# Kernel tuning notes

Measured on AMD Instinct MI355X. Metric: run time of the kernel, lower is better.

Reference implementation:

```python
import jax, jax.numpy as jnp
import numpy as np

B, S, D, HEADS = 2, 1024, 1024, 16
DK = D // HEADS           # 64: size of the 'heads' axis after split (namedtensor quirk)
LOW = D // DK             # 16: size of the contracted 'lower' axis
SCALE = float(D)          # Attention(p, scale=d_model) -> divide by d_model
NEG = -1.0e9


def setup_inputs() -> dict:
    key = jax.random.key(0)
    ks = jax.random.split(key, 8)
    query = jax.random.normal(ks[0], (B, S, D), dtype=jnp.float32)
    key_t = jax.random.normal(ks[1], (B, S, D), dtype=jnp.float32)
    value = jax.random.normal(ks[2], (B, S, D), dtype=jnp.float32)
    mask = jax.random.bernoulli(ks[3], 0.25, (B, S, S))  # True -> masked out
    std = 1.0 / np.sqrt(D)
    Wq = jax.random.normal(ks[4], (D, D), dtype=jnp.float32) * std
    Wk = jax.random.normal(ks[5], (D, D), dtype=jnp.float32) * std
    Wv = jax.random.normal(ks[6], (D, D), dtype=jnp.float32) * std
    Wo = jax.random.normal(ks[7], (D, D), dtype=jnp.float32) * std
    return {"query": query, "key": key_t, "value": value, "mask": mask,
            "Wq": Wq, "Wk": Wk, "Wv": Wv, "Wo": Wo}


def reference(query, key, value, mask, Wq, Wk, Wv, Wo):
    # nn.Linear(d_model, d_model, bias=False): y = x @ W.T
    def split(x, W):
        y = jnp.einsum('bsd,ed->bse', x, W)
        return y.reshape(B, -1, DK, LOW)  # hidden -> ('heads'=DK, 'lower'=LOW)

    q = split(query, Wq)   # [B,Sq,H,L] with H=DK, L=LOW
    k = split(key, Wk)     # [B,Sk,H,L]
    v = split(value, Wv)   # [B,Sk,H,L]

    # scores = query.dot('lower', key) / d_model  -> contract the LOW axis
    scores = jnp.einsum('bqhl,bkhl->bhqk', q, k) / SCALE
    scores = jnp.where(mask[:, None, :, :], NEG, scores)  # scores[mask] = -1e9
    p_attn = jax.nn.softmax(scores, axis=-1)  # softmax over keys; dropout=eval

    # value.dot('keys', p_attn) -> [B,H,L,Q]; stack ('heads','lower') -> hidden
    x = jnp.einsum('bkhl,bhqk->bqhl', v, p_attn).reshape(B, -1, D)
    return jnp.einsum('bsd,ed->bse', x, Wo)
```

## Files before the change

### kernel.cpp

```cpp
#include <hip/hip_runtime.h>
#include <hip/hip_bf16.h>


typedef __hip_bfloat16 bf16;
typedef __attribute__((ext_vector_type(8))) short short8;
typedef __attribute__((ext_vector_type(4))) float f32x4;
typedef __attribute__((ext_vector_type(16))) float f32x16;

__device__ __forceinline__ unsigned short f2bf(float f) {
  union { float f; unsigned u; } x; x.f = f;
  unsigned r = x.u + 0x7FFFu + ((x.u >> 16) & 1u);
  return (unsigned short)(r >> 16);
}

__device__ __forceinline__ unsigned cvt_pk_bf16(float lo, float hi) {
  unsigned r;
  asm("v_cvt_pk_bf16_f32 %0, %1, %2" : "=v"(r) : "v"(lo), "v"(hi));
  return r;
}

__device__ __forceinline__ float fast_exp2(float x) {
#if __has_builtin(__builtin_amdgcn_exp2f)
  return __builtin_amdgcn_exp2f(x);
#else
  return __expf(x * 0.6931471805599453f);
#endif
}

__global__ void detect_mask(const unsigned char* __restrict__ m, int* __restrict__ flag) {
  const int i = blockIdx.x * 256 + threadIdx.x;
  const uchar4* p = (const uchar4*)m + (size_t)i * 4;
  unsigned any = 0;
#pragma unroll
  for (int j = 0; j < 4; ++j) { uchar4 v = p[j]; any |= (unsigned)v.y | (unsigned)v.z | (unsigned)v.w; }
  if (__ballot(any != 0)) { if ((threadIdx.x & 63) == 0) atomicOr(flag, 1); }
}

__global__ void bitpack_mask(const unsigned char* __restrict__ mB, const int* __restrict__ mI,
                             const int* __restrict__ flag, unsigned* __restrict__ out) {
  const int widx = blockIdx.x * 256 + threadIdx.x;
  const int row = widx >> 5, kb = widx & 31;
  unsigned bits = 0;
  if (*flag) {
    const uchar4* p = (const uchar4*)(mB + (size_t)row * 1024 + kb * 32);
#pragma unroll
    for (int j = 0; j < 8; ++j) {
      uchar4 v = p[j];
      bits |= ((unsigned)(v.x != 0) << (4 * j)) | ((unsigned)(v.y != 0) << (4 * j + 1))
            | ((unsigned)(v.z != 0) << (4 * j + 2)) | ((unsigned)(v.w != 0) << (4 * j + 3));
    }
  } else {
    const int4* p = (const int4*)(mI + (size_t)row * 1024 + kb * 32);
#pragma unroll
    for (int j = 0; j < 8; ++j) {
      int4 v = p[j];
      bits |= ((unsigned)(v.x != 0) << (4 * j)) | ((unsigned)(v.y != 0) << (4 * j + 1))
            | ((unsigned)(v.z != 0) << (4 * j + 2)) | ((unsigned)(v.w != 0) << (4 * j + 3));
    }
  }
  const int bq = row >> 10, qb = (row & 1023) >> 5, qr = row & 31;
  out[((((bq * 32 + qb) * 8 + (kb >> 2)) * 32 + qr) << 2) + (kb & 3)] = bits;
}

__global__ void convert_all(
    const float* __restrict__ s0, const float* __restrict__ s1, const float* __restrict__ s2,
    const float* __restrict__ s3, const float* __restrict__ s4, const float* __restrict__ s5,
    const float* __restrict__ s6,
    bf16* __restrict__ d0, bf16* __restrict__ d1, bf16* __restrict__ d2,
    bf16* __restrict__ d3, bf16* __restrict__ d4, bf16* __restrict__ d5,
    bf16* __restrict__ d6) {
  const int z = blockIdx.y;
  const float* s; bf16* d; int n8; float sc = 1.0f;
  if      (z == 0) { s = s0; d = d0; n8 = 262144; }
  else if (z == 1) { s = s1; d = d1; n8 = 262144; }
  else if (z == 2) { s = s2; d = d2; n8 = 262144; }
  else if (z == 3) { s = s3; d = d3; n8 = 131072; sc = 0.0014088818758681283f; }
  else if (z == 4) { s = s4; d = d4; n8 = 131072; }
  else if (z == 5) { s = s5; d = d5; n8 = 131072; }
  else             { s = s6; d = d6; n8 = 131072; }
  const int i = blockIdx.x * 256 + threadIdx.x;
  if (i >= n8) return;
  const f32x4* p = (const f32x4*)s + (size_t)i * 2;
  f32x4 a = p[0], b = p[1];
  uint4 o;
  o.x = cvt_pk_bf16(a[0] * sc, a[1] * sc); o.y = cvt_pk_bf16(a[2] * sc, a[3] * sc);
  o.z = cvt_pk_bf16(b[0] * sc, b[1] * sc); o.w = cvt_pk_bf16(b[2] * sc, b[3] * sc);
  ((uint4*)d)[i] = o;
}

#define GSTR 40

__global__ __launch_bounds__(256) void gemm_qkv(
    const bf16* __restrict__ A0, const bf16* __restrict__ A1, const bf16* __restrict__ A2,
    const bf16* __restrict__ W0, const bf16* __restrict__ W1, const bf16* __restrict__ W2,
    bf16* __restrict__ C0, bf16* __restrict__ C1, bf16* __restrict__ C2) {
  __shared__ __align__(16) char smem[64 * 136 * 2];
  bf16* As = (bf16*)smem;
  bf16* Bs = As + 128 * GSTR;
  const int z = blockIdx.z;
  const bf16* __restrict__ A = (z == 0) ? A0 : (z == 1) ? A1 : A2;
  const bf16* __restrict__ W = (z == 0) ? W0 : (z == 1) ? W1 : W2;
  bf16* __restrict__ C = (z == 0) ? C0 : (z == 1) ? C1 : C2;
  const int tid = threadIdx.x, lane = tid & 63, w = tid >> 6;
  const int wr = (w >> 1) * 64, wc = (w & 1) * 32;
  const int row0 = blockIdx.y * 128, col0 = blockIdx.x * 64;
  const int l15 = lane & 15, kg = lane >> 4;

  f32x4 acc[4][2];
#pragma unroll
  for (int m = 0; m < 4; ++m)
#pragma unroll
    for (int n = 0; n < 2; ++n)
#pragma unroll
      for (int j = 0; j < 4; ++j) acc[m][n][j] = 0.f;

  for (int k0 = 0; k0 < 1024; k0 += 32) {
    __syncthreads();
#pragma unroll
    for (int i = 0; i < 2; ++i) {
      const int idx = i * 256 + tid, r = idx >> 2, c = idx & 3;
      *(uint4*)(&As[r * GSTR + c * 8]) = *(const uint4*)(A + (size_t)(row0 + r) * 1024 + k0 + c * 8);
    }
    {
      const int r = tid >> 2, c = tid & 3;
      *(uint4*)(&Bs[r * GSTR + c * 8]) = *(const uint4*)(W + (size_t)(col0 + r) * 1024 + k0 + c * 8);
    }
    __syncthreads();
    short8 af[4], bfr[2];
#pragma unroll
    for (int m = 0; m < 4; ++m) af[m] = *(const short8*)(&As[(wr + m * 16 + l15) * GSTR + kg * 8]);
#pragma unroll
    for (int n = 0; n < 2; ++n) bfr[n] = *(const short8*)(&Bs[(wc + n * 16 + l15) * GSTR + kg * 8]);
#pragma unroll
    for (int m = 0; m < 4; ++m)
#pragma unroll
      for (int n = 0; n < 2; ++n)
        acc[m][n] = __builtin_amdgcn_mfma_f32_16x16x32_bf16(af[m], bfr[n], acc[m][n], 0, 0, 0);
  }

  const int bb = row0 >> 10, srel0 = row0 & 1023;
  if (z == 2) {
    bf16* T = (bf16*)smem;
    __syncthreads();
#pragma unroll
    for (int m = 0; m < 4; ++m)
#pragma unroll
      for (int n = 0; n < 2; ++n) {
        const int e = wc + n * 16 + l15;
        const int rb = wr + m * 16 + kg * 4;
        uint2 u;
        u.x = cvt_pk_bf16(acc[m][n][0], acc[m][n][1]);
        u.y = cvt_pk_bf16(acc[m][n][2], acc[m][n][3]);
        *(uint2*)(T + e * 136 + rb) = u;
      }
    __syncthreads();
#pragma unroll
    for (int i = 0; i < 4; ++i) {
      const int idx = i * 256 + tid;
      const int tile = idx >> 6, within = idx & 63;
      const int hl = tile >> 2, kbl = tile & 3;
      const int e_sub = within >> 2, kq4 = within & 3;
      uint4 v = *(const uint4*)(T + (hl * 16 + e_sub) * 136 + kbl * 32 + kq4 * 8);
      const int h = (col0 >> 4) + hl;
      const size_t kb = (size_t)((srel0 >> 5) + kbl);
      *(uint4*)((unsigned short*)C + (((size_t)(bb * 64 + h) * 32 + kb) * 512 + e_sub * 32 + kq4 * 8)) = v;
    }
  } else if (z == 1) {
#pragma unroll
    for (int m = 0; m < 4; ++m)
#pragma unroll
      for (int n = 0; n < 2; ++n) {
        const int ecol = wc + n * 16 + l15;
        const int h = (col0 >> 4) + (ecol >> 4), d = ecol & 15;
#pragma unroll
        for (int j = 0; j < 4; ++j) {
          const int s = srel0 + wr + m * 16 + kg * 4 + j;
          ((unsigned short*)C)[((size_t)(bb * 64 + h) * 32 + (s >> 5)) * 512 + (s & 31) * 16 + d] =
              f2bf(acc[m][n][j]);
        }
      }
  } else {
#pragma unroll
    for (int m = 0; m < 4; ++m)
#pragma unroll
      for (int n = 0; n < 2; ++n) {
        const int col = col0 + wc + n * 16 + l15;
#pragma unroll
        for (int j = 0; j < 4; ++j) {
          const int row = row0 + wr + m * 16 + kg * 4 + j;
          ((unsigned short*)C)[(size_t)row * 1024 + col] = f2bf(acc[m][n][j]);
        }
      }
  }
}

__global__ __launch_bounds__(256) void gemm_out(
    const bf16* __restrict__ A, const bf16* __restrict__ W, float* __restrict__ C) {
  __shared__ __align__(16) char smem[(128 + 64) * GSTR * 2];
  bf16* As = (bf16*)smem;
  bf16* Bs = As + 128 * GSTR;
  const int tid = threadIdx.x, lane = tid & 63, w = tid >> 6;
  const int wr = (w >> 1) * 64, wc = (w & 1) * 32;
  const int row0 = blockIdx.y * 128, col0 = blockIdx.x * 64;
  const int l15 = lane & 15, kg = lane >> 4;

  f32x4 acc[4][2];
#pragma unroll
  for (int m = 0; m < 4; ++m)
#pragma unroll
    for (int n = 0; n < 2; ++n)
#pragma unroll
      for (int j = 0; j < 4; ++j) acc[m][n][j] = 0.f;

  for (int k0 = 0; k0 < 1024; k0 += 32) {
    __syncthreads();
#pragma unroll
    for (int i = 0; i < 2; ++i) {
      const int idx = i * 256 + tid, r = idx >> 2, c = idx & 3;
      *(uint4*)(&As[r * GSTR + c * 8]) = *(const uint4*)(A + (size_t)(row0 + r) * 1024 + k0 + c * 8);
    }
    {
      const int r = tid >> 2, c = tid & 3;
      *(uint4*)(&Bs[r * GSTR + c * 8]) = *(const uint4*)(W + (size_t)(col0 + r) * 1024 + k0 + c * 8);
    }
    __syncthreads();
    short8 af[4], bfr[2];
#pragma unroll
    for (int m = 0; m < 4; ++m) af[m] = *(const short8*)(&As[(wr + m * 16 + l15) * GSTR + kg * 8]);
#pragma unroll
    for (int n = 0; n < 2; ++n) bfr[n] = *(const short8*)(&Bs[(wc + n * 16 + l15) * GSTR + kg * 8]);
#pragma unroll
    for (int m = 0; m < 4; ++m)
#pragma unroll
      for (int n = 0; n < 2; ++n)
        acc[m][n] = __builtin_amdgcn_mfma_f32_16x16x32_bf16(af[m], bfr[n], acc[m][n], 0, 0, 0);
  }

#pragma unroll
  for (int m = 0; m < 4; ++m)
#pragma unroll
    for (int n = 0; n < 2; ++n) {
      const int col = col0 + wc + n * 16 + l15;
#pragma unroll
      for (int j = 0; j < 4; ++j) {
        const int row = row0 + wr + m * 16 + kg * 4 + j;
        C[(size_t)row * 1024 + col] = acc[m][n][j];
      }
    }
}

__global__ __launch_bounds__(256) void attn_kernel(
    const bf16* __restrict__ Qp, const bf16* __restrict__ KT, const bf16* __restrict__ VT,
    const unsigned* __restrict__ mw, bf16* __restrict__ XO) {
  __shared__ bf16 Pl[4][32 * GSTR];
  const int tid = threadIdx.x, lane = tid & 63, w = tid >> 6;
  const int hi = lane >> 5, l31 = lane & 31, l15 = lane & 15, kg = lane >> 4;
  const int h = blockIdx.y, b = blockIdx.z;
  const int qg = w >> 1, kh = w & 1;
  const int q0 = blockIdx.x * 64 + qg * 32;

  const short8 qf = *(const short8*)(Qp + ((size_t)(b * 1024 + q0 + l31)) * 1024 + h * 16 + hi * 8);
  const bf16* __restrict__ Kb = KT + ((size_t)(b * 64 + h) * 32) * 512;
  const bf16* __restrict__ Vb = VT + ((size_t)(b * 64 + h) * 32) * 512;
  const uint4* __restrict__ Mq =
      (const uint4*)mw + ((size_t)((b * 32 + (q0 >> 5)) * 8 + kh * 4)) * 32 + l31;
  const int sh4 = hi * 4;

  f32x4 acc0, acc1, sum0, sum1;
#pragma unroll
  for (int j = 0; j < 4; ++j) { acc0[j] = 0.f; acc1[j] = 0.f; sum0[j] = 0.f; sum1[j] = 0.f; }
  f32x16 Z;
#pragma unroll
  for (int i = 0; i < 16; ++i) Z[i] = 0.f;
  short8 ones;
#pragma unroll
  for (int i = 0; i < 8; ++i) ones[i] = (short)0x3F80;

  for (int kq = 0; kq < 4; ++kq) {
    const uint4 mq = Mq[kq * 32];
#pragma unroll
    for (int t = 0; t < 4; ++t) {
      const int kbg = kh * 16 + kq * 4 + t;
      const unsigned mword = ((t == 0) ? mq.x : (t == 1) ? mq.y : (t == 2) ? mq.z : mq.w) >> sh4;
      const short8 kf = *(const short8*)(Kb + (size_t)kbg * 512 + l31 * 16 + hi * 8);
      f32x16 S = __builtin_amdgcn_mfma_f32_32x32x16_bf16(kf, qf, Z, 0, 0, 0);

      bf16* pw = &Pl[w][l31 * GSTR];
#pragma unroll
      for (int g = 0; g < 4; ++g) {
        float p0, p1, p2, p3;
        p0 = (mword & (1u << (8 * g + 0))) ? 0.f : fast_exp2(S[4 * g + 0]);
        p1 = (mword & (1u << (8 * g + 1))) ? 0.f : fast_exp2(S[4 * g + 1]);
        p2 = (mword & (1u << (8 * g + 2))) ? 0.f : fast_exp2(S[4 * g + 2]);
        p3 = (mword & (1u << (8 * g + 3))) ? 0.f : fast_exp2(S[4 * g + 3]);
        uint2 u;
        u.x = cvt_pk_bf16(p0, p1);
        u.y = cvt_pk_bf16(p2, p3);
        *(uint2*)(pw + 8 * g + 4 * hi) = u;
      }

      const short8 vf = *(const short8*)(Vb + (size_t)kbg * 512 + l15 * 32 + kg * 8);
      const short8 pa0 = *(const short8*)(&Pl[w][l15 * GSTR + kg * 8]);
      const short8 pa1 = *(const short8*)(&Pl[w][(16 + l15) * GSTR + kg * 8]);
      acc0 = __builtin_amdgcn_mfma_f32_16x16x32_bf16(pa0, vf, acc0, 0, 0, 0);
      acc1 = __builtin_amdgcn_mfma_f32_16x16x32_bf16(pa1, vf, acc1, 0, 0, 0);
      sum0 = __builtin_amdgcn_mfma_f32_16x16x32_bf16(pa0, ones, sum0, 0, 0, 0);
      sum1 = __builtin_amdgcn_mfma_f32_16x16x32_bf16(pa1, ones, sum1, 0, 0, 0);
    }
  }

  float* fl = (float*)&Pl[0][0];
  __syncthreads();
  if (kh) {
    float* dst = fl + ((size_t)(qg * 64 + lane)) * 16;
#pragma unroll
    for (int j = 0; j < 4; ++j) {
      dst[j] = acc0[j]; dst[4 + j] = acc1[j]; dst[8 + j] = sum0[j]; dst[12 + j] = sum1[j];
    }
  }
  __syncthreads();
  if (!kh) {
    const float* src = fl + ((size_t)(qg * 64 + lane)) * 16;
#pragma unroll
    for (int j = 0; j < 4; ++j) {
      const float o0 = acc0[j] + src[j],      d0 = sum0[j] + src[8 + j];
      const float o1 = acc1[j] + src[4 + j],  d1 = sum1[j] + src[12 + j];
      const size_t colo = (size_t)h * 16 + l15;
      ((unsigned short*)XO)[((size_t)(b * 1024 + q0 + kg * 4 + j)) * 1024 + colo] = f2bf(o0 / d0);
      ((unsigned short*)XO)[((size_t)(b * 1024 + q0 + 16 + kg * 4 + j)) * 1024 + colo] = f2bf(o1 / d1);
    }
  }
}

extern "C" void kernel_launch(void* const* d_in, const int* in_sizes, int n_in,
                              void* d_out, int out_size, void* d_ws, size_t ws_size,
                              hipStream_t stream) {
  const float* query = (const float*)d_in[0];
  const float* key   = (const float*)d_in[1];
  const float* value = (const float*)d_in[2];
  const void*  mask  = d_in[3];
  const float* Wq = (const float*)d_in[4];
  const float* Wk = (const float*)d_in[5];
  const float* Wv = (const float*)d_in[6];
  const float* Wo = (const float*)d_in[7];
  float* out = (float*)d_out;

  char* ws = (char*)d_ws;
  const size_t MB = 1024 * 1024;
  int* flag       = (int*)ws;
  unsigned* mbits = (unsigned*)(ws + 4096);
  bf16* Qb  = (bf16*)(ws + 4096 + 262144);
  bf16* Kb  = Qb + 2 * MB;
  bf16* Vb  = Kb + 2 * MB;
  bf16* Wqb = Vb + 2 * MB;
  bf16* Wkb = Wqb + MB;
  bf16* Wvb = Wkb + MB;
  bf16* Wob = Wvb + MB;
  bf16* Qp  = Wob + MB;
  bf16* KTl = Qp + 2 * MB;
  bf16* VTl = KTl + 2 * MB;
  bf16* XO  = VTl + 2 * MB;

  hipMemsetAsync(flag, 0, 4, stream);
  detect_mask<<<dim3(512), 256, 0, stream>>>((const unsigned char*)mask, flag);
  bitpack_mask<<<dim3(256), 256, 0, stream>>>((const unsigned char*)mask, (const int*)mask,
                                              flag, mbits);
  convert_all<<<dim3(1024, 7), 256, 0, stream>>>(query, key, value, Wq, Wk, Wv, Wo,
                                                 Qb, Kb, Vb, Wqb, Wkb, Wvb, Wob);
  gemm_qkv<<<dim3(16, 16, 3), 256, 0, stream>>>(Qb, Kb, Vb, Wqb, Wkb, Wvb, Qp, KTl, VTl);
  attn_kernel<<<dim3(16, 64, 2), 256, 0, stream>>>(Qp, KTl, VTl, mbits, XO);
  gemm_out<<<dim3(16, 16), 256, 0, stream>>>(XO, Wob, out);
}
```

Baseline: 107.8 us.

## Prefetch GEMM tiles into registers with K=64 steps and unroll attention loop

Both projection GEMMs now use a K step of 64 instead of 32. The next tile's global loads are issued into registers before the MFMAs on the current shared-memory tile, then written to shared memory after a barrier. This hides global load latency behind compute and halves the number of barrier pairs, at the cost of more registers and a larger shared-memory tile. The attention kernel also loads all mask words up front and fully unrolls its 16-step key loop so the mask loads are not serialized inside it.

```diff
diff --git a/kernel.cpp b/kernel.cpp
--- a/kernel.cpp
+++ b/kernel.cpp
@@ -89,14 +89,15 @@
 }
 
 #define GSTR 40
+#define GST2 72
 
 __global__ __launch_bounds__(256) void gemm_qkv(
     const bf16* __restrict__ A0, const bf16* __restrict__ A1, const bf16* __restrict__ A2,
     const bf16* __restrict__ W0, const bf16* __restrict__ W1, const bf16* __restrict__ W2,
     bf16* __restrict__ C0, bf16* __restrict__ C1, bf16* __restrict__ C2) {
-  __shared__ __align__(16) char smem[64 * 136 * 2];
-  bf16* As = (bf16*)smem;
-  bf16* Bs = As + 128 * GSTR;
+  __shared__ __align__(16) bf16 smem[(128 + 64) * GST2];
+  bf16* As = smem;
+  bf16* Bs = smem + 128 * GST2;
   const int z = blockIdx.z;
   const bf16* __restrict__ A = (z == 0) ? A0 : (z == 1) ? A1 : A2;
   const bf16* __restrict__ W = (z == 0) ? W0 : (z == 1) ? W1 : W2;
@@ -105,6 +106,7 @@
   const int wr = (w >> 1) * 64, wc = (w & 1) * 32;
   const int row0 = blockIdx.y * 128, col0 = blockIdx.x * 64;
   const int l15 = lane & 15, kg = lane >> 4;
+  const int sr = tid >> 3, sc8 = (tid & 7) * 8;
 
   f32x4 acc[4][2];
 #pragma unroll
@@ -114,34 +116,60 @@
 #pragma unroll
       for (int j = 0; j < 4; ++j) acc[m][n][j] = 0.f;
 
-  for (int k0 = 0; k0 < 1024; k0 += 32) {
+  uint4 ga[4], gb[2];
+#pragma unroll
+  for (int i = 0; i < 4; ++i)
+    ga[i] = *(const uint4*)(A + (size_t)(row0 + i * 32 + sr) * 1024 + sc8);
+#pragma unroll
+  for (int i = 0; i < 2; ++i)
+    gb[i] = *(const uint4*)(W + (size_t)(col0 + i * 32 + sr) * 1024 + sc8);
+#pragma unroll
+  for (int i = 0; i < 4; ++i) *(uint4*)(&As[(i * 32 + sr) * GST2 + sc8]) = ga[i];
+#pragma unroll
+  for (int i = 0; i < 2; ++i) *(uint4*)(&Bs[(i * 32 + sr) * GST2 + sc8]) = gb[i];
+  __syncthreads();
+
+  for (int t = 0; t < 16; ++t) {
+    if (t < 15) {
+      const int k0 = (t + 1) * 64;
+#pragma unroll
+      for (int i = 0; i < 4; ++i)
+        ga[i] = *(const uint4*)(A + (size_t)(row0 + i * 32 + sr) * 1024 + k0 + sc8);
+#pragma unroll
+      for (int i = 0; i < 2; ++i)
+        gb[i] = *(const uint4*)(W + (size_t)(col0 + i * 32 + sr) * 1024 + k0 + sc8);
+    }
+    short8 af[4][2], bfr[2][2];
+#pragma unroll
+    for (int m = 0; m < 4; ++m)
+#pragma unroll
+      for (int ks = 0; ks < 2; ++ks)
+        af[m][ks] = *(const short8*)(&As[(wr + m * 16 + l15) * GST2 + ks * 32 + kg * 8]);
+#pragma unroll
+    for (int n = 0; n < 2; ++n)
+#pragma unroll
+      for (int ks = 0; ks < 2; ++ks)
+        bfr[n][ks] = *(const short8*)(&Bs[(wc + n * 16 + l15) * GST2 + ks * 32 + kg * 8]);
+#pragma unroll
+    for (int ks = 0; ks < 2; ++ks)
+#pragma unroll
+      for (int m = 0; m < 4; ++m)
+#pragma unroll
+        for (int n = 0; n < 2; ++n)
+          acc[m][n] = __builtin_amdgcn_mfma_f32_16x16x32_bf16(af[m][ks], bfr[n][ks], acc[m][n], 0, 0, 0);
     __syncthreads();
-#pragma unroll
-    for (int i = 0; i < 2; ++i) {
-      const int idx = i * 256 + tid, r = idx >> 2, c = idx & 3;
-      *(uint4*)(&As[r * GSTR + c * 8]) = *(const uint4*)(A + (size_t)(row0 + r) * 1024 + k0 + c * 8);
-    }
-    {
-      const int r = tid >> 2, c = tid & 3;
-      *(uint4*)(&Bs[r * GSTR + c * 8]) = *(const uint4*)(W + (size_t)(col0 + r) * 1024 + k0 + c * 8);
+    if (t < 15) {
+#pragma unroll
+      for (int i = 0; i < 4; ++i) *(uint4*)(&As[(i * 32 + sr) * GST2 + sc8]) = ga[i];
+#pragma unroll
+      for (int i = 0; i < 2; ++i) *(uint4*)(&Bs[(i * 32 + sr) * GST2 + sc8]) = gb[i];
     }
     __syncthreads();
-    short8 af[4], bfr[2];
-#pragma unroll
-    for (int m = 0; m < 4; ++m) af[m] = *(const short8*)(&As[(wr + m * 16 + l15) * GSTR + kg * 8]);
-#pragma unroll
-    for (int n = 0; n < 2; ++n) bfr[n] = *(const short8*)(&Bs[(wc + n * 16 + l15) * GSTR + kg * 8]);
-#pragma unroll
-    for (int m = 0; m < 4; ++m)
-#pragma unroll
-      for (int n = 0; n < 2; ++n)
-        acc[m][n] = __builtin_amdgcn_mfma_f32_16x16x32_bf16(af[m], bfr[n], acc[m][n], 0, 0, 0);
   }
 
   const int bb = row0 >> 10, srel0 = row0 & 1023;
   if (z == 2) {
     bf16* T = (bf16*)smem;
-    __syncthreads();
 #pragma unroll
     for (int m = 0; m < 4; ++m)
 #pragma unroll
@@ -196,13 +224,14 @@
 
 __global__ __launch_bounds__(256) void gemm_out(
     const bf16* __restrict__ A, const bf16* __restrict__ W, float* __restrict__ C) {
-  __shared__ __align__(16) char smem[(128 + 64) * GSTR * 2];
-  bf16* As = (bf16*)smem;
-  bf16* Bs = As + 128 * GSTR;
+  __shared__ __align__(16) bf16 smem[(128 + 64) * GST2];
+  bf16* As = smem;
+  bf16* Bs = smem + 128 * GST2;
   const int tid = threadIdx.x, lane = tid & 63, w = tid >> 6;
   const int wr = (w >> 1) * 64, wc = (w & 1) * 32;
   const int row0 = blockIdx.y * 128, col0 = blockIdx.x * 64;
   const int l15 = lane & 15, kg = lane >> 4;
+  const int sr = tid >> 3, sc8 = (tid & 7) * 8;
 
   f32x4 acc[4][2];
 #pragma unroll
@@ -212,28 +241,55 @@
 #pragma unroll
       for (int j = 0; j < 4; ++j) acc[m][n][j] = 0.f;
 
-  for (int k0 = 0; k0 < 1024; k0 += 32) {
+  uint4 ga[4], gb[2];
+#pragma unroll
+  for (int i = 0; i < 4; ++i)
+    ga[i] = *(const uint4*)(A + (size_t)(row0 + i * 32 + sr) * 1024 + sc8);
+#pragma unroll
+  for (int i = 0; i < 2; ++i)
+    gb[i] = *(const uint4*)(W + (size_t)(col0 + i * 32 + sr) * 1024 + sc8);
+#pragma unroll
+  for (int i = 0; i < 4; ++i) *(uint4*)(&As[(i * 32 + sr) * GST2 + sc8]) = ga[i];
+#pragma unroll
+  for (int i = 0; i < 2; ++i) *(uint4*)(&Bs[(i * 32 + sr) * GST2 + sc8]) = gb[i];
+  __syncthreads();
+
+  for (int t = 0; t < 16; ++t) {
+    if (t < 15) {
+      const int k0 = (t + 1) * 64;
+#pragma unroll
+      for (int i = 0; i < 4; ++i)
+        ga[i] = *(const uint4*)(A + (size_t)(row0 + i * 32 + sr) * 1024 + k0 + sc8);
+#pragma unroll
+      for (int i = 0; i < 2; ++i)
+        gb[i] = *(const uint4*)(W + (size_t)(col0 + i * 32 + sr) * 1024 + k0 + sc8);
+    }
+    short8 af[4][2], bfr[2][2];
+#pragma unroll
+    for (int m = 0; m < 4; ++m)
+#pragma unroll
+      for (int ks = 0; ks < 2; ++ks)
+        af[m][ks] = *(const short8*)(&As[(wr + m * 16 + l15) * GST2 + ks * 32 + kg * 8]);
+#pragma unroll
+    for (int n = 0; n < 2; ++n)
+#pragma unroll
+      for (int ks = 0; ks < 2; ++ks)
+        bfr[n][ks] = *(const short8*)(&Bs[(wc + n * 16 + l15) * GST2 + ks * 32 + kg * 8]);
+#pragma unroll
+    for (int ks = 0; ks < 2; ++ks)
+#pragma unroll
+      for (int m = 0; m < 4; ++m)
+#pragma unroll
+        for (int n = 0; n < 2; ++n)
+          acc[m][n] = __builtin_amdgcn_mfma_f32_16x16x32_bf16(af[m][ks], bfr[n][ks], acc[m][n], 0, 0, 0);
     __syncthreads();
-#pragma unroll
-    for (int i = 0; i < 2; ++i) {
-      const int idx = i * 256 + tid, r = idx >> 2, c = idx & 3;
-      *(uint4*)(&As[r * GSTR + c * 8]) = *(const uint4*)(A + (size_t)(row0 + r) * 1024 + k0 + c * 8);
-    }
-    {
-      const int r = tid >> 2, c = tid & 3;
-      *(uint4*)(&Bs[r * GSTR + c * 8]) = *(const uint4*)(W + (size_t)(col0 + r) * 1024 + k0 + c * 8);
+    if (t < 15) {
+#pragma unroll
+      for (int i = 0; i < 4; ++i) *(uint4*)(&As[(i * 32 + sr) * GST2 + sc8]) = ga[i];
+#pragma unroll
+      for (int i = 0; i < 2; ++i) *(uint4*)(&Bs[(i * 32 + sr) * GST2 + sc8]) = gb[i];
     }
     __syncthreads();
-    short8 af[4], bfr[2];
-#pragma unroll
-    for (int m = 0; m < 4; ++m) af[m] = *(const short8*)(&As[(wr + m * 16 + l15) * GSTR + kg * 8]);
-#pragma unroll
-    for (int n = 0; n < 2; ++n) bfr[n] = *(const short8*)(&Bs[(wc + n * 16 + l15) * GSTR + kg * 8]);
-#pragma unroll
-    for (int m = 0; m < 4; ++m)
-#pragma unroll
-      for (int n = 0; n < 2; ++n)
-        acc[m][n] = __builtin_amdgcn_mfma_f32_16x16x32_bf16(af[m], bfr[n], acc[m][n], 0, 0, 0);
   }
 
 #pragma unroll
@@ -266,6 +322,10 @@
       (const uint4*)mw + ((size_t)((b * 32 + (q0 >> 5)) * 8 + kh * 4)) * 32 + l31;
   const int sh4 = hi * 4;
 
+  const uint4 mqa = Mq[0], mqb = Mq[32], mqc = Mq[64], mqd = Mq[96];
+  const unsigned mm[16] = {mqa.x, mqa.y, mqa.z, mqa.w, mqb.x, mqb.y, mqb.z, mqb.w,
+                           mqc.x, mqc.y, mqc.z, mqc.w, mqd.x, mqd.y, mqd.z, mqd.w};
+
   f32x4 acc0, acc1, sum0, sum1;
 #pragma unroll
   for (int j = 0; j < 4; ++j) { acc0[j] = 0.f; acc1[j] = 0.f; sum0[j] = 0.f; sum1[j] = 0.f; }
@@ -276,37 +336,34 @@
 #pragma unroll
   for (int i = 0; i < 8; ++i) ones[i] = (short)0x3F80;
 
-  for (int kq = 0; kq < 4; ++kq) {
-    const uint4 mq = Mq[kq * 32];
-#pragma unroll
-    for (int t = 0; t < 4; ++t) {
-      const int kbg = kh * 16 + kq * 4 + t;
-      const unsigned mword = ((t == 0) ? mq.x : (t == 1) ? mq.y : (t == 2) ? mq.z : mq.w) >> sh4;
-      const short8 kf = *(const short8*)(Kb + (size_t)kbg * 512 + l31 * 16 + hi * 8);
-      f32x16 S = __builtin_amdgcn_mfma_f32_32x32x16_bf16(kf, qf, Z, 0, 0, 0);
-
-      bf16* pw = &Pl[w][l31 * GSTR];
-#pragma unroll
-      for (int g = 0; g < 4; ++g) {
-        float p0, p1, p2, p3;
-        p0 = (mword & (1u << (8 * g + 0))) ? 0.f : fast_exp2(S[4 * g + 0]);
-        p1 = (mword & (1u << (8 * g + 1))) ? 0.f : fast_exp2(S[4 * g + 1]);
-        p2 = (mword & (1u << (8 * g + 2))) ? 0.f : fast_exp2(S[4 * g + 2]);
-        p3 = (mword & (1u << (8 * g + 3))) ? 0.f : fast_exp2(S[4 * g + 3]);
-        uint2 u;
-        u.x = cvt_pk_bf16(p0, p1);
-        u.y = cvt_pk_bf16(p2, p3);
-        *(uint2*)(pw + 8 * g + 4 * hi) = u;
-      }
-
-      const short8 vf = *(const short8*)(Vb + (size_t)kbg * 512 + l15 * 32 + kg * 8);
-      const short8 pa0 = *(const short8*)(&Pl[w][l15 * GSTR + kg * 8]);
-      const short8 pa1 = *(const short8*)(&Pl[w][(16 + l15) * GSTR + kg * 8]);
-      acc0 = __builtin_amdgcn_mfma_f32_16x16x32_bf16(pa0, vf, acc0, 0, 0, 0);
-      acc1 = __builtin_amdgcn_mfma_f32_16x16x32_bf16(pa1, vf, acc1, 0, 0, 0);
-      sum0 = __builtin_amdgcn_mfma_f32_16x16x32_bf16(pa0, ones, sum0, 0, 0, 0);
-      sum1 = __builtin_amdgcn_mfma_f32_16x16x32_bf16(pa1, ones, sum1, 0, 0, 0);
-    }
+#pragma unroll
+  for (int t = 0; t < 16; ++t) {
+    const int kbg = kh * 16 + t;
+    const unsigned mword = mm[t] >> sh4;
+    const short8 kf = *(const short8*)(Kb + (size_t)kbg * 512 + l31 * 16 + hi * 8);
+    f32x16 S = __builtin_amdgcn_mfma_f32_32x32x16_bf16(kf, qf, Z, 0, 0, 0);
+
+    bf16* pw = &Pl[w][l31 * GSTR];
+#pragma unroll
+    for (int g = 0; g < 4; ++g) {
+      float p0, p1, p2, p3;
+      p0 = (mword & (1u << (8 * g + 0))) ? 0.f : fast_exp2(S[4 * g + 0]);
+      p1 = (mword & (1u << (8 * g + 1))) ? 0.f : fast_exp2(S[4 * g + 1]);
+      p2 = (mword & (1u << (8 * g + 2))) ? 0.f : fast_exp2(S[4 * g + 2]);
+      p3 = (mword & (1u << (8 * g + 3))) ? 0.f : fast_exp2(S[4 * g + 3]);
+      uint2 u;
+      u.x = cvt_pk_bf16(p0, p1);
+      u.y = cvt_pk_bf16(p2, p3);
+      *(uint2*)(pw + 8 * g + 4 * hi) = u;
+    }
+
+    const short8 vf = *(const short8*)(Vb + (size_t)kbg * 512 + l15 * 32 + kg * 8);
+    const short8 pa0 = *(const short8*)(&Pl[w][l15 * GSTR + kg * 8]);
+    const short8 pa1 = *(const short8*)(&Pl[w][(16 + l15) * GSTR + kg * 8]);
+    acc0 = __builtin_amdgcn_mfma_f32_16x16x32_bf16(pa0, vf, acc0, 0, 0, 0);
+    acc1 = __builtin_amdgcn_mfma_f32_16x16x32_bf16(pa1, vf, acc1, 0, 0, 0);
+    sum0 = __builtin_amdgcn_mfma_f32_16x16x32_bf16(pa0, ones, sum0, 0, 0, 0);
+    sum1 = __builtin_amdgcn_mfma_f32_16x16x32_bf16(pa1, ones, sum1, 0, 0, 0);
   }
 
   float* fl = (float*)&Pl[0][0];
```

Result: slower. 173.4 us (+60.9%).
